# Kernel optimization log

Measured on AMD Instinct MI355X. Metric: run time of the kernel, lower is better.

The kernel has to match this reference:

```python
import jax, jax.numpy as jnp
import numpy as np

S, U, NMEL, T = 32, 10, 40, 120
H, D = 768, 256


def setup_inputs() -> dict:
    key = jax.random.key(0)
    ks = jax.random.split(key, 16)
    def p(k, shape, scale=0.03):
        return jax.random.normal(k, shape, jnp.float32) * scale
    inp = {"mel": jax.random.normal(ks[0], (S, U, 1, NMEL, T), jnp.float32)}
    in_sizes = [NMEL, H, H]
    for l in range(3):
        inp[f"Wih{l}"] = p(ks[1 + 4 * l], (4 * H, in_sizes[l]))
        inp[f"Whh{l}"] = p(ks[2 + 4 * l], (4 * H, H))
        inp[f"bih{l}"] = p(ks[3 + 4 * l], (4 * H,))
        inp[f"bhh{l}"] = p(ks[4 + 4 * l], (4 * H,))
    inp["Wproj"] = p(ks[13], (D, H))
    inp["bproj"] = p(ks[14], (D,))
    inp["loss_w"] = jnp.array([10.0], jnp.float32)
    inp["loss_b"] = jnp.array([-5.0], jnp.float32)
    return inp


def _lstm_layer(x, Wih, Whh, bih, bhh):
    # x: (B, T, In) -> (B, T, H). PyTorch gate order: i, f, g, o.
    B = x.shape[0]
    Hh = Whh.shape[1]
    h0 = jnp.zeros((B, Hh), x.dtype)
    c0 = jnp.zeros((B, Hh), x.dtype)
    bias = bih + bhh
    def step(carry, xt):
        h, c = carry
        gates = xt @ Wih.T + h @ Whh.T + bias  # (B, 4H)
        i, f, g, o = jnp.split(gates, 4, axis=-1)
        c = jax.nn.sigmoid(f) * c + jax.nn.sigmoid(i) * jnp.tanh(g)
        h = jax.nn.sigmoid(o) * jnp.tanh(c)
        return (h, c), h
    _, hs = jax.lax.scan(step, (h0, c0), jnp.swapaxes(x, 0, 1))  # (T, B, H)
    return jnp.swapaxes(hs, 0, 1)


def _ge2e(d3, w, b):
    # d3: (S, U, D) unit-norm d-vectors; w, b: (1,) scalars.
    s, u, _ = d3.shape
    cent = d3.mean(axis=1)  # (S, D) per-speaker centroids
    # leave-one-out positive centroid: (U*cent - self) / (U-1)
    pos_cent = (cent[:, None, :] * u - d3) / (u - 1)  # (S, U, D)
    # cosine sim with eps=1e-6 (F.cosine_similarity clamps norms)
    na = jnp.maximum(jnp.linalg.norm(d3, axis=-1), 1e-6)
    npc = jnp.maximum(jnp.linalg.norm(pos_cent, axis=-1), 1e-6)
    pos_cos = jnp.sum(d3 * pos_cent, axis=-1) / (na * npc)  # (S, U)
    pos_sim = w[0] * pos_cos + b[0]
    # negative sims vs other speakers' centroids (eps=1e-8 default)
    nd = jnp.maximum(jnp.linalg.norm(d3, axis=-1), 1e-8)  # (S, U)
    nc = jnp.maximum(jnp.linalg.norm(cent, axis=-1), 1e-8)  # (S,)
    all_cos = jnp.einsum('sud,kd->suk', d3, cent) / (nd[..., None] * nc[None, None, :])
    jj = jnp.arange(s - 1)
    idx = jj[None, :] + (jj[None, :] >= jnp.arange(s)[:, None])  # (S, S-1), skips own speaker
    neg_cos = jnp.take_along_axis(all_cos, jnp.broadcast_to(idx[:, None, :], (s, u, s - 1)), axis=2)
    neg_sim = w[0] * neg_cos + b[0]
    # softmax GE2E loss: -pos + log sum exp(neg)
    loss = jnp.mean(-pos_sim + jax.scipy.special.logsumexp(neg_sim, axis=2))
    return loss, pos_sim.mean(), neg_sim.mean()


def reference(mel, Wih0, Whh0, bih0, bhh0, Wih1, Whh1, bih1, bhh1,
              Wih2, Whh2, bih2, bhh2, Wproj, bproj, loss_w, loss_b):
    s, u = mel.shape[0], mel.shape[1]
    x = mel.reshape(s * u, mel.shape[3], mel.shape[4])  # (B, 40, T)
    x = jnp.transpose(x, (0, 2, 1))  # (B, T, 40)
    for (Wih, Whh, bih, bhh) in ((Wih0, Whh0, bih0, bhh0),
                                 (Wih1, Whh1, bih1, bhh1),
                                 (Wih2, Whh2, bih2, bhh2)):
        x = _lstm_layer(x, Wih, Whh, bih, bhh)
    h = x[:, -1, :]  # last time step
    dvec = h @ Wproj.T + bproj
    dvec = dvec / jnp.linalg.norm(dvec, axis=1, keepdims=True)
    d3 = dvec.reshape(s, u, -1)
    return _ge2e(d3, loss_w, loss_b)
```

## Files before the change

### kernel.cpp

```cpp
#include <hip/hip_runtime.h>
#include <math.h>

#define S_    32
#define U_    10
#define B_    320
#define T_    120
#define NMEL_ 40
#define H_    768
#define G4_   3072
#define D_    256
#define XP_   64
#define K0_   (XP_ + H_)
#define K12_  (2 * H_)
#define NP_   4

#define NB0   48
#define NB12  96
#define NBLK  (NB0 + 2 * NB12)

#define SMEM_BYTES 159744

typedef _Float16 half8 __attribute__((ext_vector_type(8)));
typedef float floatx4 __attribute__((ext_vector_type(4)));

__device__ __forceinline__ float sigm(float x) {
  return 1.f / (1.f + __expf(-x));
}
__device__ __forceinline__ float tanh_f(float x) {
  x = fminf(15.f, fmaxf(-15.f, x));
  float e = __expf(2.f * x);
  return (e - 1.f) / (e + 1.f);
}

template <int AUX>
__device__ __forceinline__ void dma16(const void* g, void* l) {
  __builtin_amdgcn_global_load_lds(
      (const __attribute__((address_space(1))) unsigned int*)g,
      (__attribute__((address_space(3))) unsigned int*)l, 16, 0, AUX);
}

template <int N>
__device__ __forceinline__ void waitvm() {
  __builtin_amdgcn_s_waitcnt(0x3FF0 | (N & 0xF) | ((N >> 4) << 14));
}


__global__ void prep_x0(const float* __restrict__ mel, _Float16* __restrict__ x0) {
  int idx = blockIdx.x * 256 + threadIdx.x;
  if (idx >= B_ * T_ * XP_) return;
  int k = idx & (XP_ - 1);
  int t = (idx >> 6) % T_;
  int b = idx / (XP_ * T_);
  float v = (k < NMEL_) ? mel[((size_t)b * NMEL_ + k) * T_ + t] : 0.f;
  x0[idx] = (_Float16)v;
}

__global__ void prep_w0(const float* __restrict__ Wih, const float* __restrict__ Whh,
                        _Float16* __restrict__ Wc) {
  int idx = blockIdx.x * 256 + threadIdx.x;
  if (idx >= G4_ * K0_) return;
  int k = idx % K0_;
  int n = idx / K0_;
  float v = 0.f;
  if (k < NMEL_)      v = Wih[(size_t)n * NMEL_ + k];
  else if (k >= XP_)  v = Whh[(size_t)n * H_ + (k - XP_)];
  Wc[idx] = (_Float16)v;
}

__global__ void prep_w12(const float* __restrict__ Wih, const float* __restrict__ Whh,
                         _Float16* __restrict__ Wc) {
  int idx = blockIdx.x * 256 + threadIdx.x;
  if (idx >= G4_ * K12_) return;
  int k = idx % K12_;
  int n = idx / K12_;
  float v = (k < H_) ? Wih[(size_t)n * H_ + k] : Whh[(size_t)n * H_ + (k - H_)];
  Wc[idx] = (_Float16)v;
}

__global__ void prep_bias(const float* __restrict__ bih, const float* __restrict__ bhh,
                          float* __restrict__ bias) {
  int idx = blockIdx.x * 256 + threadIdx.x;
  if (idx < G4_) bias[idx] = bih[idx] + bhh[idx];
}


__device__ __forceinline__ void wait_group(int* fl, int sp, int lp, int lane) {
  if (lp < 0 || lp > 2) return;
  if (sp < lp || sp > lp + T_ - 1) return;
  const int tgt = (lp == 0) ? NB0 : NB12;
  const int base = (sp * 3 + lp) * 96;
  int spin = 0;
  for (;;) {
    int v0 = (lane < tgt)
                 ? __hip_atomic_load(&fl[base + lane], __ATOMIC_RELAXED,
                                     __HIP_MEMORY_SCOPE_AGENT) : 1;
    int v1 = (lane + 64 < tgt)
                 ? __hip_atomic_load(&fl[base + 64 + lane], __ATOMIC_RELAXED,
                                     __HIP_MEMORY_SCOPE_AGENT) : 1;
    if (__all(v0 != 0 && v1 != 0)) break;
    __builtin_amdgcn_s_sleep(1);
    if (++spin > 2000000) break;
  }
}

template <int NT, int NSTG, int NC, int AUX>
__device__ __forceinline__ void gemm_phase(
    const _Float16* __restrict__ lwW, int wchunk0, _Float16* __restrict__ lwA,
    const char* __restrict__ src, int strideE,
    int m0, int lane, floatx4 (&acc)[2][NT]) {
  const int lr = lane & 15, quad = lane >> 4;
  const int rrow = lane >> 2, rq = lane & 3;
  const int rqs = rq ^ ((rrow >> 1) & 3);
  const size_t o0 = ((size_t)(m0 + rrow) * strideE + rqs * 8) * 2;
  const size_t o1 = ((size_t)(m0 + 16 + rrow) * strideE + rqs * 8) * 2;

  auto issue = [&](int c) {
    const int slot = c % NSTG;
    char* ld = (char*)lwA + ((size_t)slot * 320 + m0) * 64;
    const char* g = src + (size_t)c * 64;
    dma16<AUX>(g + o0, ld);
    dma16<AUX>(g + o1, ld + 1024);
  };

#pragma unroll
  for (int p = 0; p < (NSTG < NC ? NSTG : NC); ++p) issue(p);

  const int asw = (quad ^ ((lr >> 1) & 3)) * 8;

#pragma unroll
  for (int c = 0; c < NC; ++c) {
    const int rem = NC - 1 - c;
    if (rem >= NSTG - 1)      waitvm<2 * (NSTG - 1)>();
    else if (rem == 1)        waitvm<2>();
    else                      waitvm<0>();
    const int slot = c % NSTG;
    const _Float16* aB = lwA + ((size_t)slot * 320 + m0 + lr) * 32 + asw;
    half8 a0 = *(const half8*)(aB);
    half8 a1 = *(const half8*)(aB + 16 * 32);
    half8 bf[NT];
#pragma unroll
    for (int nt = 0; nt < NT; ++nt)
      bf[nt] = *(const half8*)(lwW +
               ((size_t)((wchunk0 + c) * NT * 16 + nt * 16 + lr) * 32 + asw));
#pragma unroll
    for (int nt = 0; nt < NT; ++nt) {
      acc[0][nt] = __builtin_amdgcn_mfma_f32_16x16x32_f16(a0, bf[nt], acc[0][nt], 0, 0, 0);
      acc[1][nt] = __builtin_amdgcn_mfma_f32_16x16x32_f16(a1, bf[nt], acc[1][nt], 0, 0, 0);
    }
    if (c + NSTG < NC) issue(c + NSTG);
  }
}

__global__ __launch_bounds__(640)
void lstm_persist(const _Float16* __restrict__ x0,
                  const _Float16* __restrict__ Wc0, const _Float16* __restrict__ Wc1,
                  const _Float16* __restrict__ Wc2,
                  const float* __restrict__ bias, _Float16* __restrict__ hbuf,
                  int* __restrict__ flags, int* __restrict__ tick,
                  int* __restrict__ leadDone) {
  extern __shared__ _Float16 lw[];
  const int bid = blockIdx.x;

  int layer, tile, units, K;
  const _Float16* Wsrc;
  if (bid < NB0)            { layer = 0; tile = bid;              units = 16; K = K0_;  Wsrc = Wc0; }
  else if (bid < NB0+NB12)  { layer = 1; tile = bid - NB0;        units = 8;  K = K12_; Wsrc = Wc1; }
  else                      { layer = 2; tile = bid - NB0 - NB12; units = 8;  K = K12_; Wsrc = Wc2; }
  const int nrows = units * 4;
  const int j0 = tile * units;
  _Float16* lwA = lw + (size_t)(K / 32) * nrows * 32;

  unsigned xcc;
  asm volatile("s_getreg_b32 %0, hwreg(HW_REG_XCC_ID)" : "=s"(xcc));
  xcc &= 7;

  {
    const int total = (K / 32) * nrows * 4;
    for (int idx = threadIdx.x; idx < total; idx += 640) {
      int c = idx / (nrows * 4);
      int rem = idx % (nrows * 4);
      int r = rem >> 2;
      int q = rem & 3;
      int grow = (r / units) * H_ + j0 + (r % units);
      half8 v = *(const half8*)(Wsrc + (size_t)grow * K + c * 32 + q * 8);
      int qs = q ^ ((r >> 1) & 3);
      *(half8*)(lw + ((size_t)(c * nrows + r) * 32 + qs * 8)) = v;
    }
  }
  __syncthreads();

  const int lane = threadIdx.x & 63;
  const int wv = threadIdx.x >> 6;
  const int lr = lane & 15;
  const int quad = lane >> 4;
  const int m0 = wv * 32;
  const int m1 = wv * 32 + 16;
  const int j = j0 + ((units == 16) ? lr : (lr & 7));

  const float bI = bias[layer * G4_ + 0 * H_ + j];
  const float bF = bias[layer * G4_ + 1 * H_ + j];
  const float bG = bias[layer * G4_ + 2 * H_ + j];
  const float bO = bias[layer * G4_ + 3 * H_ + j];

  float cst[2][4] = {{0.f, 0.f, 0.f, 0.f}, {0.f, 0.f, 0.f, 0.f}};

  for (int t = 0; t < T_; ++t) {
    const int s = layer + t;
    const int pprev = (s - 1) & (NP_ - 1);
    const int pcur = s & (NP_ - 1);
    const _Float16* hown = hbuf + (size_t)(layer * NP_ + pprev) * B_ * H_;
    _Float16* hout = hbuf + (size_t)(layer * NP_ + pcur) * B_ * H_;

    if (threadIdx.x == 0) {
      if (__hip_atomic_fetch_add(&tick[xcc * 128 + s], 1, __ATOMIC_RELAXED,
                                 __HIP_MEMORY_SCOPE_AGENT) == 0) {
        __builtin_amdgcn_fence(__ATOMIC_ACQUIRE, "agent");
        __hip_atomic_store(&leadDone[xcc * 128 + s], 1, __ATOMIC_RELEASE,
                           __HIP_MEMORY_SCOPE_AGENT);
      }
    }
    if (lane == 0) {
      int spin = 0;
      while (__hip_atomic_load(&leadDone[xcc * 128 + s], __ATOMIC_RELAXED,
                               __HIP_MEMORY_SCOPE_AGENT) == 0) {
        __builtin_amdgcn_s_sleep(1);
        if (++spin > 2000000) break;
      }
    }

    floatx4 acc0[2][4];
    floatx4 acc2[2][2];

    if (layer == 0) {
#pragma unroll
      for (int a = 0; a < 2; ++a)
#pragma unroll
        for (int b = 0; b < 4; ++b) acc0[a][b] = (floatx4){0.f, 0.f, 0.f, 0.f};
      const char* xsrc = (const char*)(x0 + (size_t)t * XP_);
      gemm_phase<4, 2, 2, 0>(lw, 0, lwA, xsrc, T_ * XP_, m0, lane, acc0);
      wait_group(flags, s - 1, 0, lane);
      gemm_phase<4, 2, 24, 1>(lw, 2, lwA, (const char*)hown, H_, m0, lane, acc0);
    } else {
      wait_group(flags, s - 1, layer - 1, lane);
#pragma unroll
      for (int a = 0; a < 2; ++a)
#pragma unroll
        for (int b = 0; b < 2; ++b) acc2[a][b] = (floatx4){0.f, 0.f, 0.f, 0.f};
      const char* xsrc = (const char*)(hbuf + (size_t)((layer - 1) * NP_ + pprev) * B_ * H_);
      gemm_phase<2, 3, 24, 1>(lw, 0, lwA, xsrc, H_, m0, lane, acc2);
      wait_group(flags, s - 1, layer, lane);
      gemm_phase<2, 3, 24, 1>(lw, 24, lwA, (const char*)hown, H_, m0, lane, acc2);
    }

    wait_group(flags, s - 3, layer + 1, lane);

    if (layer == 0) {
#pragma unroll
      for (int mt = 0; mt < 2; ++mt)
#pragma unroll
        for (int r = 0; r < 4; ++r) {
          float iv = acc0[mt][0][r] + bI;
          float fv = acc0[mt][1][r] + bF;
          float gv = acc0[mt][2][r] + bG;
          float ov = acc0[mt][3][r] + bO;
          float cn = sigm(fv) * cst[mt][r] + sigm(iv) * tanh_f(gv);
          cst[mt][r] = cn;
          int m = (mt ? m1 : m0) + quad * 4 + r;
          hout[(size_t)m * H_ + j] = (_Float16)(sigm(ov) * tanh_f(cn));
        }
    } else {
#pragma unroll
      for (int mt = 0; mt < 2; ++mt)
#pragma unroll
        for (int r = 0; r < 4; ++r) {
          float t0 = acc2[mt][0][r], t1 = acc2[mt][1][r];
          float p0 = __shfl_xor(t0, 8, 64);
          float p1 = __shfl_xor(t1, 8, 64);
          bool lo = (lr < 8);
          float iv = (lo ? t0 : p0) + bI;
          float fv = (lo ? p0 : t0) + bF;
          float gv = (lo ? t1 : p1) + bG;
          float ov = (lo ? p1 : t1) + bO;
          float cn = sigm(fv) * cst[mt][r] + sigm(iv) * tanh_f(gv);
          cst[mt][r] = cn;
          if (lo) {
            int m = (mt ? m1 : m0) + quad * 4 + r;
            hout[(size_t)m * H_ + j] = (_Float16)(sigm(ov) * tanh_f(cn));
          }
        }
    }

    __syncthreads();
    if (threadIdx.x == 0)
      __hip_atomic_store(&flags[(s * 3 + layer) * 96 + tile], 1, __ATOMIC_RELEASE,
                         __HIP_MEMORY_SCOPE_AGENT);
  }
}

__global__ void dvec_kernel(const _Float16* __restrict__ hlast, const float* __restrict__ Wproj,
                            const float* __restrict__ bproj, float* __restrict__ d3) {
  const int m = blockIdx.x;
  const int d = threadIdx.x;
  const _Float16* h = hlast + (size_t)m * H_;
  const float* w = Wproj + (size_t)d * H_;
  float acc = bproj[d];
  for (int k = 0; k < H_; k++) acc += (float)h[k] * w[k];
  __shared__ float red[256];
  red[d] = acc * acc;
  __syncthreads();
  for (int off = 128; off > 0; off >>= 1) {
    if (d < off) red[d] += red[d + off];
    __syncthreads();
  }
  float nrm = sqrtf(red[0]);
  d3[(size_t)m * D_ + d] = acc / nrm;
}

__device__ float block_reduce_sum(float x, float* red) {
  const int d = threadIdx.x;
  red[d] = x;
  __syncthreads();
  for (int off = 128; off > 0; off >>= 1) {
    if (d < off) red[d] += red[d + off];
    __syncthreads();
  }
  float r = red[0];
  __syncthreads();
  return r;
}

__global__ void cent_kernel(const float* __restrict__ d3, float* __restrict__ cent,
                            float* __restrict__ ncent) {
  const int sIdx = blockIdx.x;
  const int d = threadIdx.x;
  float acc = 0.f;
  for (int u = 0; u < U_; u++) acc += d3[((size_t)sIdx * U_ + u) * D_ + d];
  acc *= (1.f / U_);
  cent[sIdx * D_ + d] = acc;
  __shared__ float red[256];
  float n2 = block_reduce_sum(acc * acc, red);
  if (d == 0) ncent[sIdx] = fmaxf(sqrtf(n2), 1e-8f);
}

__global__ void ge2e_kernel(const float* __restrict__ d3, const float* __restrict__ cent,
                            const float* __restrict__ ncent, const float* __restrict__ loss_w,
                            const float* __restrict__ loss_b, float* __restrict__ accums) {
  const int p = blockIdx.x;
  const int sIdx = p / U_;
  const int d = threadIdx.x;
  __shared__ float red[256];
  __shared__ float sims[S_];

  const float v = d3[(size_t)p * D_ + d];
  const float cs = cent[sIdx * D_ + d];
  const float pc = (cs * U_ - v) * (1.f / (U_ - 1));

  float nv2 = block_reduce_sum(v * v, red);
  float npc2 = block_reduce_sum(pc * pc, red);
  float dotp = block_reduce_sum(v * pc, red);

  const float w = loss_w[0], b = loss_b[0];
  const float na = fmaxf(sqrtf(nv2), 1e-6f);
  const float npc = fmaxf(sqrtf(npc2), 1e-6f);
  const float pos_sim = w * (dotp / (na * npc)) + b;
  const float nd = fmaxf(sqrtf(nv2), 1e-8f);

  for (int k = 0; k < S_; k++) {
    float dk = block_reduce_sum(v * cent[k * D_ + d], red);
    if (d == 0) sims[k] = w * (dk / (nd * ncent[k])) + b;
  }
  __syncthreads();
  if (d == 0) {
    float mx = -1e30f;
    for (int k = 0; k < S_; k++)
      if (k != sIdx) mx = fmaxf(mx, sims[k]);
    float se = 0.f, sn = 0.f;
    for (int k = 0; k < S_; k++)
      if (k != sIdx) { se += expf(sims[k] - mx); sn += sims[k]; }
    float lse = mx + logf(se);
    atomicAdd(&accums[0], -pos_sim + lse);
    atomicAdd(&accums[1], pos_sim);
    atomicAdd(&accums[2], sn);
  }
}

__global__ void finalize_kernel(const float* __restrict__ accums, float* __restrict__ out) {
  if (threadIdx.x == 0) {
    out[0] = accums[0] / (float)(S_ * U_);
    out[1] = accums[1] / (float)(S_ * U_);
    out[2] = accums[2] / (float)(S_ * U_ * (S_ - 1));
  }
}

extern "C" void kernel_launch(void* const* d_in, const int* in_sizes, int n_in,
                              void* d_out, int out_size, void* d_ws, size_t ws_size,
                              hipStream_t stream) {
  const float* mel = (const float*)d_in[0];
  const float* Wih[3] = {(const float*)d_in[1], (const float*)d_in[5], (const float*)d_in[9]};
  const float* Whh[3] = {(const float*)d_in[2], (const float*)d_in[6], (const float*)d_in[10]};
  const float* bih[3] = {(const float*)d_in[3], (const float*)d_in[7], (const float*)d_in[11]};
  const float* bhh[3] = {(const float*)d_in[4], (const float*)d_in[8], (const float*)d_in[12]};
  const float* Wproj = (const float*)d_in[13];
  const float* bproj = (const float*)d_in[14];
  const float* loss_w = (const float*)d_in[15];
  const float* loss_b = (const float*)d_in[16];
  float* out = (float*)d_out;

  char* ws = (char*)d_ws;
  size_t off = 0;
  auto alloc = [&](size_t bytes) -> void* {
    void* p = ws + off;
    off = (off + bytes + 255) & ~(size_t)255;
    return p;
  };
  _Float16* x0   = (_Float16*)alloc((size_t)B_ * T_ * XP_ * 2);
  _Float16* Wc0  = (_Float16*)alloc((size_t)G4_ * K0_ * 2);
  _Float16* Wc1  = (_Float16*)alloc((size_t)G4_ * K12_ * 2);
  _Float16* Wc2  = (_Float16*)alloc((size_t)G4_ * K12_ * 2);
  float*    bias = (float*)alloc((size_t)3 * G4_ * 4);
  _Float16* hbuf = (_Float16*)alloc((size_t)3 * NP_ * B_ * H_ * 2);
  float*    d3   = (float*)alloc((size_t)B_ * D_ * 4);
  float*    cent = (float*)alloc((size_t)S_ * D_ * 4);
  float*    ncent = (float*)alloc((size_t)S_ * 4);
  float*    accums = (float*)alloc(64);
  int*      flags = (int*)alloc((size_t)(T_ + 3) * 3 * 96 * 4);
  int*      tick  = (int*)alloc((size_t)8 * 128 * 4);
  int*      lead  = (int*)alloc((size_t)8 * 128 * 4);

  hipMemsetAsync(hbuf, 0, (size_t)3 * NP_ * B_ * H_ * 2, stream);
  hipMemsetAsync(accums, 0, 64, stream);
  hipMemsetAsync(flags, 0, (size_t)(T_ + 3) * 3 * 96 * 4, stream);
  hipMemsetAsync(tick, 0, (size_t)8 * 128 * 4, stream);
  hipMemsetAsync(lead, 0, (size_t)8 * 128 * 4, stream);

  prep_x0<<<(B_ * T_ * XP_ + 255) / 256, 256, 0, stream>>>(mel, x0);
  prep_w0<<<(G4_ * K0_ + 255) / 256, 256, 0, stream>>>(Wih[0], Whh[0], Wc0);
  prep_w12<<<(G4_ * K12_ + 255) / 256, 256, 0, stream>>>(Wih[1], Whh[1], Wc1);
  prep_w12<<<(G4_ * K12_ + 255) / 256, 256, 0, stream>>>(Wih[2], Whh[2], Wc2);
  for (int l = 0; l < 3; l++)
    prep_bias<<<(G4_ + 255) / 256, 256, 0, stream>>>(bih[l], bhh[l], bias + l * G4_);

  hipFuncSetAttribute((const void*)lstm_persist,
                      hipFuncAttributeMaxDynamicSharedMemorySize, SMEM_BYTES);
  void* kargs[] = {(void*)&x0, (void*)&Wc0, (void*)&Wc1, (void*)&Wc2,
                   (void*)&bias, (void*)&hbuf, (void*)&flags, (void*)&tick,
                   (void*)&lead};
  hipLaunchCooperativeKernel((const void*)lstm_persist, dim3(NBLK), dim3(640),
                             kargs, SMEM_BYTES, stream);

  const _Float16* hlast = hbuf + (size_t)(2 * NP_ + 1) * B_ * H_;
  dvec_kernel<<<B_, 256, 0, stream>>>(hlast, Wproj, bproj, d3);
  cent_kernel<<<S_, 256, 0, stream>>>(d3, cent, ncent);
  ge2e_kernel<<<B_, 256, 0, stream>>>(d3, cent, ncent, loss_w, loss_b, accums);
  finalize_kernel<<<1, 64, 0, stream>>>(accums, out);
}
```

Measured before the change: 3.341 ms.

## Load activation tiles directly into registers instead of LDS DMA staging

Replaces the global_load_lds DMA staging of the activation (A) operand with direct global_load_dwordx4 into a register ring buffer (depth 4 or 5, sc0 for coherent h reads), so the MFMA fragments come straight from registers. This removes the LDS A-staging area, reducing the shared-memory request, and adds a launch-bounds occupancy hint of 3. The cost is more VGPR pressure and loads that no longer use the swizzled LDS layout, so the global access pattern per lane changes.

```diff
diff --git a/kernel.cpp b/kernel.cpp
--- a/kernel.cpp
+++ b/kernel.cpp
@@ -18,7 +18,7 @@
 #define NB12  96
 #define NBLK  (NB0 + 2 * NB12)
 
-#define SMEM_BYTES 159744
+#define SMEM_BYTES 106496
 
 typedef _Float16 half8 __attribute__((ext_vector_type(8)));
 typedef float floatx4 __attribute__((ext_vector_type(4)));
@@ -32,16 +32,19 @@
   return (e - 1.f) / (e + 1.f);
 }
 
-template <int AUX>
-__device__ __forceinline__ void dma16(const void* g, void* l) {
-  __builtin_amdgcn_global_load_lds(
-      (const __attribute__((address_space(1))) unsigned int*)g,
-      (__attribute__((address_space(3))) unsigned int*)l, 16, 0, AUX);
-}
-
 template <int N>
 __device__ __forceinline__ void waitvm() {
   __builtin_amdgcn_s_waitcnt(0x3FF0 | (N & 0xF) | ((N >> 4) << 14));
+}
+
+template <bool SC0>
+__device__ __forceinline__ half8 aload(const _Float16* p) {
+  half8 d;
+  if constexpr (SC0)
+    asm volatile("global_load_dwordx4 %0, %1, off sc0" : "=v"(d) : "v"(p));
+  else
+    asm volatile("global_load_dwordx4 %0, %1, off" : "=v"(d) : "v"(p));
+  return d;
 }
 
 
@@ -103,40 +106,36 @@
   }
 }
 
-template <int NT, int NSTG, int NC, int AUX>
+template <int NT, int D, int NC, bool SC0>
 __device__ __forceinline__ void gemm_phase(
-    const _Float16* __restrict__ lwW, int wchunk0, _Float16* __restrict__ lwA,
-    const char* __restrict__ src, int strideE,
+    const _Float16* __restrict__ lwW, int wchunk0,
+    const _Float16* __restrict__ src, int strideE,
     int m0, int lane, floatx4 (&acc)[2][NT]) {
   const int lr = lane & 15, quad = lane >> 4;
-  const int rrow = lane >> 2, rq = lane & 3;
-  const int rqs = rq ^ ((rrow >> 1) & 3);
-  const size_t o0 = ((size_t)(m0 + rrow) * strideE + rqs * 8) * 2;
-  const size_t o1 = ((size_t)(m0 + 16 + rrow) * strideE + rqs * 8) * 2;
-
-  auto issue = [&](int c) {
-    const int slot = c % NSTG;
-    char* ld = (char*)lwA + ((size_t)slot * 320 + m0) * 64;
-    const char* g = src + (size_t)c * 64;
-    dma16<AUX>(g + o0, ld);
-    dma16<AUX>(g + o1, ld + 1024);
-  };
-
-#pragma unroll
-  for (int p = 0; p < (NSTG < NC ? NSTG : NC); ++p) issue(p);
+  const _Float16* a0p = src + (size_t)(m0 + lr) * strideE + quad * 8;
+  const _Float16* a1p = a0p + (size_t)16 * strideE;
+
+  constexpr int DD = (D < NC) ? D : NC;
+  half8 abuf[DD][2];
+#pragma unroll
+  for (int p = 0; p < DD; ++p) {
+    abuf[p][0] = aload<SC0>(a0p + (size_t)p * 32);
+    abuf[p][1] = aload<SC0>(a1p + (size_t)p * 32);
+  }
 
   const int asw = (quad ^ ((lr >> 1) & 3)) * 8;
 
 #pragma unroll
   for (int c = 0; c < NC; ++c) {
     const int rem = NC - 1 - c;
-    if (rem >= NSTG - 1)      waitvm<2 * (NSTG - 1)>();
+    if (rem >= DD - 1)        waitvm<2 * (DD - 1)>();
+    else if (rem == 3)        waitvm<6>();
+    else if (rem == 2)        waitvm<4>();
     else if (rem == 1)        waitvm<2>();
     else                      waitvm<0>();
-    const int slot = c % NSTG;
-    const _Float16* aB = lwA + ((size_t)slot * 320 + m0 + lr) * 32 + asw;
-    half8 a0 = *(const half8*)(aB);
-    half8 a1 = *(const half8*)(aB + 16 * 32);
+    __builtin_amdgcn_sched_barrier(0);
+    half8 a0 = abuf[c % DD][0];
+    half8 a1 = abuf[c % DD][1];
     half8 bf[NT];
 #pragma unroll
     for (int nt = 0; nt < NT; ++nt)
@@ -147,11 +146,14 @@
       acc[0][nt] = __builtin_amdgcn_mfma_f32_16x16x32_f16(a0, bf[nt], acc[0][nt], 0, 0, 0);
       acc[1][nt] = __builtin_amdgcn_mfma_f32_16x16x32_f16(a1, bf[nt], acc[1][nt], 0, 0, 0);
     }
-    if (c + NSTG < NC) issue(c + NSTG);
-  }
-}
-
-__global__ __launch_bounds__(640)
+    if (c + DD < NC) {
+      abuf[c % DD][0] = aload<SC0>(a0p + (size_t)(c + DD) * 32);
+      abuf[c % DD][1] = aload<SC0>(a1p + (size_t)(c + DD) * 32);
+    }
+  }
+}
+
+__global__ __launch_bounds__(640, 3)
 void lstm_persist(const _Float16* __restrict__ x0,
                   const _Float16* __restrict__ Wc0, const _Float16* __restrict__ Wc1,
                   const _Float16* __restrict__ Wc2,
@@ -168,7 +170,6 @@
   else                      { layer = 2; tile = bid - NB0 - NB12; units = 8;  K = K12_; Wsrc = Wc2; }
   const int nrows = units * 4;
   const int j0 = tile * units;
-  _Float16* lwA = lw + (size_t)(K / 32) * nrows * 32;
 
   unsigned xcc;
   asm volatile("s_getreg_b32 %0, hwreg(HW_REG_XCC_ID)" : "=s"(xcc));
@@ -236,20 +237,19 @@
       for (int a = 0; a < 2; ++a)
 #pragma unroll
         for (int b = 0; b < 4; ++b) acc0[a][b] = (floatx4){0.f, 0.f, 0.f, 0.f};
-      const char* xsrc = (const char*)(x0 + (size_t)t * XP_);
-      gemm_phase<4, 2, 2, 0>(lw, 0, lwA, xsrc, T_ * XP_, m0, lane, acc0);
+      gemm_phase<4, 4, 2, false>(lw, 0, x0 + (size_t)t * XP_, T_ * XP_, m0, lane, acc0);
       wait_group(flags, s - 1, 0, lane);
-      gemm_phase<4, 2, 24, 1>(lw, 2, lwA, (const char*)hown, H_, m0, lane, acc0);
+      gemm_phase<4, 4, 24, true>(lw, 2, hown, H_, m0, lane, acc0);
     } else {
       wait_group(flags, s - 1, layer - 1, lane);
 #pragma unroll
       for (int a = 0; a < 2; ++a)
 #pragma unroll
         for (int b = 0; b < 2; ++b) acc2[a][b] = (floatx4){0.f, 0.f, 0.f, 0.f};
-      const char* xsrc = (const char*)(hbuf + (size_t)((layer - 1) * NP_ + pprev) * B_ * H_);
-      gemm_phase<2, 3, 24, 1>(lw, 0, lwA, xsrc, H_, m0, lane, acc2);
+      const _Float16* xsrc = hbuf + (size_t)((layer - 1) * NP_ + pprev) * B_ * H_;
+      gemm_phase<2, 5, 24, true>(lw, 0, xsrc, H_, m0, lane, acc2);
       wait_group(flags, s - 1, layer, lane);
-      gemm_phase<2, 3, 24, 1>(lw, 24, lwA, (const char*)hown, H_, m0, lane, acc2);
+      gemm_phase<2, 5, 24, true>(lw, 24, hown, H_, m0, lane, acc2);
     }
 
     wait_group(flags, s - 3, layer + 1, lane);
```

New measurement: 4.774 ms. 1.43x slower.

## Halve layer 1-2 block count and stream recurrent weights from global memory

Applied to the files above, without the earlier changes.

Layers 1 and 2 now use 48 blocks of 16 hidden units each instead of 96 blocks of 8, matching layer 0 and using the full 4-tile MFMA width. This removes the shuffle-based gate gather and cuts the number of blocks that must synchronise per step. Each block now has twice the weight rows, which no longer fit in LDS. So the input-weight half stays in LDS while the recurrent-weight half is pre-tiled by a new prep kernel and streamed from global/L2 into registers inside a new pipelined GEMM loop. The trade-off is fewer CUs doing the recurrence and extra global weight traffic on the critical recurrent path every timestep.

```diff
diff --git a/kernel.cpp b/kernel.cpp
--- a/kernel.cpp
+++ b/kernel.cpp
@@ -14,11 +14,11 @@
 #define K12_  (2 * H_)
 #define NP_   4
 
-#define NB0   48
-#define NB12  96
-#define NBLK  (NB0 + 2 * NB12)
+#define NB_   48
+#define NBLK  (3 * NB_)
 
 #define SMEM_BYTES 159744
+#define WLDS12 24
 
 typedef _Float16 half8 __attribute__((ext_vector_type(8)));
 typedef float floatx4 __attribute__((ext_vector_type(4)));
@@ -42,6 +42,12 @@
 template <int N>
 __device__ __forceinline__ void waitvm() {
   __builtin_amdgcn_s_waitcnt(0x3FF0 | (N & 0xF) | ((N >> 4) << 14));
+}
+
+__device__ __forceinline__ half8 aload(const _Float16* p) {
+  half8 d;
+  asm volatile("global_load_dwordx4 %0, %1, off" : "=v"(d) : "v"(p));
+  return d;
 }
 
 
@@ -83,21 +89,37 @@
   if (idx < G4_) bias[idx] = bih[idx] + bhh[idx];
 }
 
+__global__ void prep_wtile(const float* __restrict__ Whh1, const float* __restrict__ Whh2,
+                           _Float16* __restrict__ Wt) {
+  int idx = blockIdx.x * 256 + threadIdx.x;
+  const int total = 2 * NB_ * 24 * 64 * 4;
+  if (idx >= total) return;
+  int g = idx & 3;
+  int r = (idx >> 2) & 63;
+  int rest = idx >> 8;
+  int ci = rest % 24;
+  int rest2 = rest / 24;
+  int tile = rest2 % NB_;
+  int l2 = rest2 / NB_;
+  const float* Whh = l2 ? Whh2 : Whh1;
+  int n = (r >> 4) * H_ + tile * 16 + (r & 15);
+  int k = ci * 32 + g * 8;
+  _Float16 tmp[8];
+  for (int u = 0; u < 8; ++u) tmp[u] = (_Float16)Whh[(size_t)n * H_ + k + u];
+  *(half8*)(Wt + (((((size_t)l2 * NB_ + tile) * 24 + ci) * 64 + r) * 32 + g * 8)) = *(half8*)tmp;
+}
+
 
 __device__ __forceinline__ void wait_group(int* fl, int sp, int lp, int lane) {
   if (lp < 0 || lp > 2) return;
   if (sp < lp || sp > lp + T_ - 1) return;
-  const int tgt = (lp == 0) ? NB0 : NB12;
   const int base = (sp * 3 + lp) * 96;
   int spin = 0;
   for (;;) {
-    int v0 = (lane < tgt)
+    int v0 = (lane < NB_)
                  ? __hip_atomic_load(&fl[base + lane], __ATOMIC_RELAXED,
                                      __HIP_MEMORY_SCOPE_AGENT) : 1;
-    int v1 = (lane + 64 < tgt)
-                 ? __hip_atomic_load(&fl[base + 64 + lane], __ATOMIC_RELAXED,
-                                     __HIP_MEMORY_SCOPE_AGENT) : 1;
-    if (__all(v0 != 0 && v1 != 0)) break;
+    if (__all(v0 != 0)) break;
     __builtin_amdgcn_s_sleep(1);
     if (++spin > 2000000) break;
   }
@@ -151,40 +173,92 @@
   }
 }
 
+template <int NSTG, int NC>
+__device__ __forceinline__ void gemm_ws(
+    _Float16* __restrict__ lwA,
+    const char* __restrict__ src, int strideE,
+    const _Float16* __restrict__ wt,
+    int m0, int lane, floatx4 (&acc)[2][4]) {
+  const int lr = lane & 15, quad = lane >> 4;
+  const int rrow = lane >> 2, rq = lane & 3;
+  const int rqs = rq ^ ((rrow >> 1) & 3);
+  const size_t o0 = ((size_t)(m0 + rrow) * strideE + rqs * 8) * 2;
+  const size_t o1 = ((size_t)(m0 + 16 + rrow) * strideE + rqs * 8) * 2;
+  const _Float16* wbase = wt + (size_t)lr * 32 + quad * 8;
+
+  half8 wbuf[NSTG][4];
+
+  auto issue = [&](int c) {
+    const int slot = c % NSTG;
+    char* ld = (char*)lwA + ((size_t)slot * 320 + m0) * 64;
+    const char* g = src + (size_t)c * 64;
+    dma16<1>(g + o0, ld);
+    dma16<1>(g + o1, ld + 1024);
+    const _Float16* wp = wbase + (size_t)c * 64 * 32;
+#pragma unroll
+    for (int nt = 0; nt < 4; ++nt)
+      wbuf[slot][nt] = aload(wp + nt * 16 * 32);
+  };
+
+#pragma unroll
+  for (int p = 0; p < (NSTG < NC ? NSTG : NC); ++p) issue(p);
+
+  const int asw = (quad ^ ((lr >> 1) & 3)) * 8;
+
+#pragma unroll
+  for (int c = 0; c < NC; ++c) {
+    const int rem = NC - 1 - c;
+    if (rem >= NSTG - 1)      waitvm<6 * (NSTG - 1)>();
+    else if (rem == 1)        waitvm<6>();
+    else                      waitvm<0>();
+    __builtin_amdgcn_sched_barrier(0);
+    const int slot = c % NSTG;
+    const _Float16* aB = lwA + ((size_t)slot * 320 + m0 + lr) * 32 + asw;
+    half8 a0 = *(const half8*)(aB);
+    half8 a1 = *(const half8*)(aB + 16 * 32);
+#pragma unroll
+    for (int nt = 0; nt < 4; ++nt) {
+      acc[0][nt] = __builtin_amdgcn_mfma_f32_16x16x32_f16(a0, wbuf[slot][nt], acc[0][nt], 0, 0, 0);
+      acc[1][nt] = __builtin_amdgcn_mfma_f32_16x16x32_f16(a1, wbuf[slot][nt], acc[1][nt], 0, 0, 0);
+    }
+    if (c + NSTG < NC) issue(c + NSTG);
+  }
+}
+
 __global__ __launch_bounds__(640)
 void lstm_persist(const _Float16* __restrict__ x0,
                   const _Float16* __restrict__ Wc0, const _Float16* __restrict__ Wc1,
-                  const _Float16* __restrict__ Wc2,
+                  const _Float16* __restrict__ Wc2, const _Float16* __restrict__ Wt,
                   const float* __restrict__ bias, _Float16* __restrict__ hbuf,
                   int* __restrict__ flags, int* __restrict__ tick,
                   int* __restrict__ leadDone) {
   extern __shared__ _Float16 lw[];
   const int bid = blockIdx.x;
 
-  int layer, tile, units, K;
+  int layer, tile, wlds, K;
   const _Float16* Wsrc;
-  if (bid < NB0)            { layer = 0; tile = bid;              units = 16; K = K0_;  Wsrc = Wc0; }
-  else if (bid < NB0+NB12)  { layer = 1; tile = bid - NB0;        units = 8;  K = K12_; Wsrc = Wc1; }
-  else                      { layer = 2; tile = bid - NB0 - NB12; units = 8;  K = K12_; Wsrc = Wc2; }
-  const int nrows = units * 4;
-  const int j0 = tile * units;
-  _Float16* lwA = lw + (size_t)(K / 32) * nrows * 32;
+  if (bid < NB_)            { layer = 0; tile = bid;           wlds = 26;     K = K0_;  Wsrc = Wc0; }
+  else if (bid < 2 * NB_)   { layer = 1; tile = bid - NB_;     wlds = WLDS12; K = K12_; Wsrc = Wc1; }
+  else                      { layer = 2; tile = bid - 2 * NB_; wlds = WLDS12; K = K12_; Wsrc = Wc2; }
+  const int j0 = tile * 16;
+  _Float16* lwA = lw + (size_t)wlds * 64 * 32;
+  const _Float16* wt = Wt + ((size_t)((layer - 1) * NB_ + tile) * 24) * 64 * 32;
 
   unsigned xcc;
   asm volatile("s_getreg_b32 %0, hwreg(HW_REG_XCC_ID)" : "=s"(xcc));
   xcc &= 7;
 
   {
-    const int total = (K / 32) * nrows * 4;
+    const int total = wlds * 64 * 4;
     for (int idx = threadIdx.x; idx < total; idx += 640) {
-      int c = idx / (nrows * 4);
-      int rem = idx % (nrows * 4);
+      int c = idx >> 8;
+      int rem = idx & 255;
       int r = rem >> 2;
       int q = rem & 3;
-      int grow = (r / units) * H_ + j0 + (r % units);
+      int grow = (r >> 4) * H_ + j0 + (r & 15);
       half8 v = *(const half8*)(Wsrc + (size_t)grow * K + c * 32 + q * 8);
       int qs = q ^ ((r >> 1) & 3);
-      *(half8*)(lw + ((size_t)(c * nrows + r) * 32 + qs * 8)) = v;
+      *(half8*)(lw + ((size_t)(c * 64 + r) * 32 + qs * 8)) = v;
     }
   }
   __syncthreads();
@@ -195,7 +269,7 @@
   const int quad = lane >> 4;
   const int m0 = wv * 32;
   const int m1 = wv * 32 + 16;
-  const int j = j0 + ((units == 16) ? lr : (lr & 7));
+  const int j = j0 + lr;
 
   const float bI = bias[layer * G4_ + 0 * H_ + j];
   const float bF = bias[layer * G4_ + 1 * H_ + j];
@@ -229,66 +303,39 @@
     }
 
     floatx4 acc0[2][4];
-    floatx4 acc2[2][2];
+#pragma unroll
+    for (int a = 0; a < 2; ++a)
+#pragma unroll
+      for (int b = 0; b < 4; ++b) acc0[a][b] = (floatx4){0.f, 0.f, 0.f, 0.f};
 
     if (layer == 0) {
-#pragma unroll
-      for (int a = 0; a < 2; ++a)
-#pragma unroll
-        for (int b = 0; b < 4; ++b) acc0[a][b] = (floatx4){0.f, 0.f, 0.f, 0.f};
       const char* xsrc = (const char*)(x0 + (size_t)t * XP_);
       gemm_phase<4, 2, 2, 0>(lw, 0, lwA, xsrc, T_ * XP_, m0, lane, acc0);
       wait_group(flags, s - 1, 0, lane);
       gemm_phase<4, 2, 24, 1>(lw, 2, lwA, (const char*)hown, H_, m0, lane, acc0);
     } else {
       wait_group(flags, s - 1, layer - 1, lane);
-#pragma unroll
-      for (int a = 0; a < 2; ++a)
-#pragma unroll
-        for (int b = 0; b < 2; ++b) acc2[a][b] = (floatx4){0.f, 0.f, 0.f, 0.f};
       const char* xsrc = (const char*)(hbuf + (size_t)((layer - 1) * NP_ + pprev) * B_ * H_);
-      gemm_phase<2, 3, 24, 1>(lw, 0, lwA, xsrc, H_, m0, lane, acc2);
+      gemm_phase<4, 3, 24, 1>(lw, 0, lwA, xsrc, H_, m0, lane, acc0);
       wait_group(flags, s - 1, layer, lane);
-      gemm_phase<2, 3, 24, 1>(lw, 24, lwA, (const char*)hown, H_, m0, lane, acc2);
+      gemm_ws<3, 24>(lwA, (const char*)hown, H_, wt, m0, lane, acc0);
     }
 
     wait_group(flags, s - 3, layer + 1, lane);
 
-    if (layer == 0) {
-#pragma unroll
-      for (int mt = 0; mt < 2; ++mt)
-#pragma unroll
-        for (int r = 0; r < 4; ++r) {
-          float iv = acc0[mt][0][r] + bI;
-          float fv = acc0[mt][1][r] + bF;
-          float gv = acc0[mt][2][r] + bG;
-          float ov = acc0[mt][3][r] + bO;
-          float cn = sigm(fv) * cst[mt][r] + sigm(iv) * tanh_f(gv);
-          cst[mt][r] = cn;
-          int m = (mt ? m1 : m0) + quad * 4 + r;
-          hout[(size_t)m * H_ + j] = (_Float16)(sigm(ov) * tanh_f(cn));
-        }
-    } else {
-#pragma unroll
-      for (int mt = 0; mt < 2; ++mt)
-#pragma unroll
-        for (int r = 0; r < 4; ++r) {
-          float t0 = acc2[mt][0][r], t1 = acc2[mt][1][r];
-          float p0 = __shfl_xor(t0, 8, 64);
-          float p1 = __shfl_xor(t1, 8, 64);
-          bool lo = (lr < 8);
-          float iv = (lo ? t0 : p0) + bI;
-          float fv = (lo ? p0 : t0) + bF;
-          float gv = (lo ? t1 : p1) + bG;
-          float ov = (lo ? p1 : t1) + bO;
-          float cn = sigm(fv) * cst[mt][r] + sigm(iv) * tanh_f(gv);
-          cst[mt][r] = cn;
-          if (lo) {
-            int m = (mt ? m1 : m0) + quad * 4 + r;
-            hout[(size_t)m * H_ + j] = (_Float16)(sigm(ov) * tanh_f(cn));
-          }
-        }
-    }
+#pragma unroll
+    for (int mt = 0; mt < 2; ++mt)
+#pragma unroll
+      for (int r = 0; r < 4; ++r) {
+        float iv = acc0[mt][0][r] + bI;
+        float fv = acc0[mt][1][r] + bF;
+        float gv = acc0[mt][2][r] + bG;
+        float ov = acc0[mt][3][r] + bO;
+        float cn = sigm(fv) * cst[mt][r] + sigm(iv) * tanh_f(gv);
+        cst[mt][r] = cn;
+        int m = (mt ? m1 : m0) + quad * 4 + r;
+        hout[(size_t)m * H_ + j] = (_Float16)(sigm(ov) * tanh_f(cn));
+      }
 
     __syncthreads();
     if (threadIdx.x == 0)
@@ -417,6 +464,7 @@
   _Float16* Wc0  = (_Float16*)alloc((size_t)G4_ * K0_ * 2);
   _Float16* Wc1  = (_Float16*)alloc((size_t)G4_ * K12_ * 2);
   _Float16* Wc2  = (_Float16*)alloc((size_t)G4_ * K12_ * 2);
+  _Float16* Wt   = (_Float16*)alloc((size_t)2 * NB_ * 24 * 64 * 32 * 2);
   float*    bias = (float*)alloc((size_t)3 * G4_ * 4);
   _Float16* hbuf = (_Float16*)alloc((size_t)3 * NP_ * B_ * H_ * 2);
   float*    d3   = (float*)alloc((size_t)B_ * D_ * 4);
@@ -437,12 +485,13 @@
   prep_w0<<<(G4_ * K0_ + 255) / 256, 256, 0, stream>>>(Wih[0], Whh[0], Wc0);
   prep_w12<<<(G4_ * K12_ + 255) / 256, 256, 0, stream>>>(Wih[1], Whh[1], Wc1);
   prep_w12<<<(G4_ * K12_ + 255) / 256, 256, 0, stream>>>(Wih[2], Whh[2], Wc2);
+  prep_wtile<<<(2 * NB_ * 24 * 64 * 4 + 255) / 256, 256, 0, stream>>>(Whh[1], Whh[2], Wt);
   for (int l = 0; l < 3; l++)
     prep_bias<<<(G4_ + 255) / 256, 256, 0, stream>>>(bih[l], bhh[l], bias + l * G4_);
 
   hipFuncSetAttribute((const void*)lstm_persist,
                       hipFuncAttributeMaxDynamicSharedMemorySize, SMEM_BYTES);
-  void* kargs[] = {(void*)&x0, (void*)&Wc0, (void*)&Wc1, (void*)&Wc2,
+  void* kargs[] = {(void*)&x0, (void*)&Wc0, (void*)&Wc1, (void*)&Wc2, (void*)&Wt,
                    (void*)&bias, (void*)&hbuf, (void*)&flags, (void*)&tick,
                    (void*)&lead};
   hipLaunchCooperativeKernel((const void*)lstm_persist, dim3(NBLK), dim3(640),
```

Measured after the change: 5.938 ms. +77.7%, slower.

## Merge input and recurrent GEMM phases into one pipelined loop; drop per-XCC tick barrier

Applied to the files above, without the earlier changes.

Merges the two GEMM phases per timestep (input projection and recurrent h) into one software-pipelined loop. The dependency wait on the previous step's h is placed just before the first recurrent chunk is prefetched, so the pipeline no longer drains and refills at the phase boundary. Also removes the per-XCC leader tick/leadDone handshake each step, and recurrent loads now use a different cache-policy aux value (17). Risks: losing whatever locality or co-scheduling the XCC gating gave, and correctness depends on the flag waits alone ordering the data.

```diff
diff --git a/kernel.cpp b/kernel.cpp
--- a/kernel.cpp
+++ b/kernel.cpp
@@ -103,27 +103,37 @@
   }
 }
 
-template <int NT, int NSTG, int NC, int AUX>
-__device__ __forceinline__ void gemm_phase(
-    const _Float16* __restrict__ lwW, int wchunk0, _Float16* __restrict__ lwA,
-    const char* __restrict__ src, int strideE,
-    int m0, int lane, floatx4 (&acc)[2][NT]) {
+template <int NT, int NSTG, int NC, int CSPLIT, int AUXX>
+__device__ __forceinline__ void gemm_merged(
+    const _Float16* __restrict__ lwW, _Float16* __restrict__ lwA,
+    const char* __restrict__ srcX, int strideX,
+    const char* __restrict__ srcH, int strideH,
+    int m0, int lane, floatx4 (&acc)[2][NT],
+    int* __restrict__ flags, int sprev, int layer) {
   const int lr = lane & 15, quad = lane >> 4;
   const int rrow = lane >> 2, rq = lane & 3;
   const int rqs = rq ^ ((rrow >> 1) & 3);
-  const size_t o0 = ((size_t)(m0 + rrow) * strideE + rqs * 8) * 2;
-  const size_t o1 = ((size_t)(m0 + 16 + rrow) * strideE + rqs * 8) * 2;
+  const size_t ox0 = ((size_t)(m0 + rrow) * strideX + rqs * 8) * 2;
+  const size_t ox1 = ((size_t)(m0 + 16 + rrow) * strideX + rqs * 8) * 2;
+  const size_t oh0 = ((size_t)(m0 + rrow) * strideH + rqs * 8) * 2;
+  const size_t oh1 = ((size_t)(m0 + 16 + rrow) * strideH + rqs * 8) * 2;
 
   auto issue = [&](int c) {
     const int slot = c % NSTG;
     char* ld = (char*)lwA + ((size_t)slot * 320 + m0) * 64;
-    const char* g = src + (size_t)c * 64;
-    dma16<AUX>(g + o0, ld);
-    dma16<AUX>(g + o1, ld + 1024);
+    if (c < CSPLIT) {
+      const char* g = srcX + (size_t)c * 64;
+      dma16<AUXX>(g + ox0, ld);
+      dma16<AUXX>(g + ox1, ld + 1024);
+    } else {
+      const char* g = srcH + (size_t)(c - CSPLIT) * 64;
+      dma16<17>(g + oh0, ld);
+      dma16<17>(g + oh1, ld + 1024);
+    }
   };
 
 #pragma unroll
-  for (int p = 0; p < (NSTG < NC ? NSTG : NC); ++p) issue(p);
+  for (int p = 0; p < NSTG; ++p) issue(p);
 
   const int asw = (quad ^ ((lr >> 1) & 3)) * 8;
 
@@ -141,13 +151,17 @@
 #pragma unroll
     for (int nt = 0; nt < NT; ++nt)
       bf[nt] = *(const half8*)(lwW +
-               ((size_t)((wchunk0 + c) * NT * 16 + nt * 16 + lr) * 32 + asw));
+               ((size_t)(c * NT * 16 + nt * 16 + lr) * 32 + asw));
 #pragma unroll
     for (int nt = 0; nt < NT; ++nt) {
       acc[0][nt] = __builtin_amdgcn_mfma_f32_16x16x32_f16(a0, bf[nt], acc[0][nt], 0, 0, 0);
       acc[1][nt] = __builtin_amdgcn_mfma_f32_16x16x32_f16(a1, bf[nt], acc[1][nt], 0, 0, 0);
     }
-    if (c + NSTG < NC) issue(c + NSTG);
+    if (c + NSTG < NC) {
+      if (c + NSTG == CSPLIT)
+        wait_group(flags, sprev, layer, lane);
+      issue(c + NSTG);
+    }
   }
 }
 
@@ -156,8 +170,7 @@
                   const _Float16* __restrict__ Wc0, const _Float16* __restrict__ Wc1,
                   const _Float16* __restrict__ Wc2,
                   const float* __restrict__ bias, _Float16* __restrict__ hbuf,
-                  int* __restrict__ flags, int* __restrict__ tick,
-                  int* __restrict__ leadDone) {
+                  int* __restrict__ flags) {
   extern __shared__ _Float16 lw[];
   const int bid = blockIdx.x;
 
@@ -169,10 +182,6 @@
   const int nrows = units * 4;
   const int j0 = tile * units;
   _Float16* lwA = lw + (size_t)(K / 32) * nrows * 32;
-
-  unsigned xcc;
-  asm volatile("s_getreg_b32 %0, hwreg(HW_REG_XCC_ID)" : "=s"(xcc));
-  xcc &= 7;
 
   {
     const int total = (K / 32) * nrows * 4;
@@ -211,23 +220,6 @@
     const _Float16* hown = hbuf + (size_t)(layer * NP_ + pprev) * B_ * H_;
     _Float16* hout = hbuf + (size_t)(layer * NP_ + pcur) * B_ * H_;
 
-    if (threadIdx.x == 0) {
-      if (__hip_atomic_fetch_add(&tick[xcc * 128 + s], 1, __ATOMIC_RELAXED,
-                                 __HIP_MEMORY_SCOPE_AGENT) == 0) {
-        __builtin_amdgcn_fence(__ATOMIC_ACQUIRE, "agent");
-        __hip_atomic_store(&leadDone[xcc * 128 + s], 1, __ATOMIC_RELEASE,
-                           __HIP_MEMORY_SCOPE_AGENT);
-      }
-    }
-    if (lane == 0) {
-      int spin = 0;
-      while (__hip_atomic_load(&leadDone[xcc * 128 + s], __ATOMIC_RELAXED,
-                               __HIP_MEMORY_SCOPE_AGENT) == 0) {
-        __builtin_amdgcn_s_sleep(1);
-        if (++spin > 2000000) break;
-      }
-    }
-
     floatx4 acc0[2][4];
     floatx4 acc2[2][2];
 
@@ -236,10 +228,9 @@
       for (int a = 0; a < 2; ++a)
 #pragma unroll
         for (int b = 0; b < 4; ++b) acc0[a][b] = (floatx4){0.f, 0.f, 0.f, 0.f};
-      const char* xsrc = (const char*)(x0 + (size_t)t * XP_);
-      gemm_phase<4, 2, 2, 0>(lw, 0, lwA, xsrc, T_ * XP_, m0, lane, acc0);
-      wait_group(flags, s - 1, 0, lane);
-      gemm_phase<4, 2, 24, 1>(lw, 2, lwA, (const char*)hown, H_, m0, lane, acc0);
+      gemm_merged<4, 2, 26, 2, 0>(lw, lwA,
+          (const char*)(x0 + (size_t)t * XP_), T_ * XP_,
+          (const char*)hown, H_, m0, lane, acc0, flags, s - 1, 0);
     } else {
       wait_group(flags, s - 1, layer - 1, lane);
 #pragma unroll
@@ -247,9 +238,8 @@
 #pragma unroll
         for (int b = 0; b < 2; ++b) acc2[a][b] = (floatx4){0.f, 0.f, 0.f, 0.f};
       const char* xsrc = (const char*)(hbuf + (size_t)((layer - 1) * NP_ + pprev) * B_ * H_);
-      gemm_phase<2, 3, 24, 1>(lw, 0, lwA, xsrc, H_, m0, lane, acc2);
-      wait_group(flags, s - 1, layer, lane);
-      gemm_phase<2, 3, 24, 1>(lw, 24, lwA, (const char*)hown, H_, m0, lane, acc2);
+      gemm_merged<2, 3, 48, 24, 17>(lw, lwA,
+          xsrc, H_, (const char*)hown, H_, m0, lane, acc2, flags, s - 1, layer);
     }
 
     wait_group(flags, s - 3, layer + 1, lane);
@@ -424,14 +414,10 @@
   float*    ncent = (float*)alloc((size_t)S_ * 4);
   float*    accums = (float*)alloc(64);
   int*      flags = (int*)alloc((size_t)(T_ + 3) * 3 * 96 * 4);
-  int*      tick  = (int*)alloc((size_t)8 * 128 * 4);
-  int*      lead  = (int*)alloc((size_t)8 * 128 * 4);
 
   hipMemsetAsync(hbuf, 0, (size_t)3 * NP_ * B_ * H_ * 2, stream);
   hipMemsetAsync(accums, 0, 64, stream);
   hipMemsetAsync(flags, 0, (size_t)(T_ + 3) * 3 * 96 * 4, stream);
-  hipMemsetAsync(tick, 0, (size_t)8 * 128 * 4, stream);
-  hipMemsetAsync(lead, 0, (size_t)8 * 128 * 4, stream);
 
   prep_x0<<<(B_ * T_ * XP_ + 255) / 256, 256, 0, stream>>>(mel, x0);
   prep_w0<<<(G4_ * K0_ + 255) / 256, 256, 0, stream>>>(Wih[0], Whh[0], Wc0);
@@ -443,8 +429,7 @@
   hipFuncSetAttribute((const void*)lstm_persist,
                       hipFuncAttributeMaxDynamicSharedMemorySize, SMEM_BYTES);
   void* kargs[] = {(void*)&x0, (void*)&Wc0, (void*)&Wc1, (void*)&Wc2,
-                   (void*)&bias, (void*)&hbuf, (void*)&flags, (void*)&tick,
-                   (void*)&lead};
+                   (void*)&bias, (void*)&hbuf, (void*)&flags};
   hipLaunchCooperativeKernel((const void*)lstm_persist, dim3(NBLK), dim3(640),
                              kargs, SMEM_BYTES, stream);
 
```

Result: slower. 3.637 ms (+8.8%).
